# Kernel tuning notes

Hardware: AMD Instinct MI355X
Metric: run time of the kernel (lower is better)

The kernel has to match this reference:

```python
import jax, jax.numpy as jnp
import numpy as np

N_EXPERTS = 4
N_MODULES = 4
TOP_K = 2


def setup_inputs() -> dict:
    key = jax.random.key(0)
    k1, k2, k3 = jax.random.split(key, 3)
    B, d_model = 32768, 1024
    pooled_hidden = jax.random.normal(k1, (B, d_model), dtype=jnp.float32)
    # Xavier-uniform-ish scale for linear weights (torch Linear weight layout [out, in])
    lim_g = float(np.sqrt(6.0 / (d_model + d_model)))
    lim_r = float(np.sqrt(6.0 / (d_model + N_MODULES)))
    Wg = jax.random.uniform(k2, (d_model, d_model), jnp.float32, -lim_g, lim_g)
    Wr = jax.random.uniform(k3, (N_MODULES, d_model), jnp.float32, -lim_r, lim_r)
    return {"pooled_hidden": pooled_hidden, "Wg": Wg, "Wr": Wr}


def reference(pooled_hidden, Wg, Wr):
    # gated = g(h) = h @ Wg^T ; logits = gated @ Wr^T ; probs = softmax over modules
    gated = jnp.einsum("bd,ed->be", pooled_hidden, Wg)            # [B, d_model]
    logits = jnp.einsum("bd,md->bm", gated, Wr)                   # [B, n_modules]
    probs = jax.nn.softmax(logits, axis=-1)                        # [B, n_modules]

    # Vectorized replacement of the per-sample threshold loop:
    # prob > 0.5 -> first k experts get 1/k; else first max(1, k//2) get 1/that.
    n_lo = max(1, TOP_K // 2)
    eids = jnp.arange(N_EXPERTS)
    w_hi = jnp.where(eids < TOP_K, 1.0 / TOP_K, 0.0).astype(jnp.float32)   # [E]
    w_lo = jnp.where(eids < n_lo, 1.0 / n_lo, 0.0).astype(jnp.float32)     # [E]
    mask_hi = probs > 0.5                                          # [B, M]
    weights = jnp.where(mask_hi[:, :, None], w_hi, w_lo)          # [B, M, E]

    # Return per-module expert weights (Q, K, V, O order), each [B, n_experts]
    w = jnp.transpose(weights, (1, 0, 2))                          # [M, B, E]
    return (w[0], w[1], w[2], w[3])
```

## Files before the change

kernel.cpp:

```cpp
#include <hip/hip_runtime.h>

#define D_MODEL 1024
#define N_MOD   4
#define EB      32
#define ECHUNK  32
#define EPW     8

typedef float fx4 __attribute__((ext_vector_type(4)));

__global__ __launch_bounds__(256) void weff_partial_kernel(
    const fx4* __restrict__ Wg4,
    const float* __restrict__ Wr,
    fx4* __restrict__ partial4)
{
    const int t    = threadIdx.x;
    const int esub = t >> 6;
    const int d4   = t & 63;
    const int eb   = blockIdx.x;
    const int dc   = blockIdx.y;
    const int d4g  = dc * 64 + d4;
    const int e0   = eb * ECHUNK + esub * EPW;

    fx4 acc[N_MOD];
    #pragma unroll
    for (int m = 0; m < N_MOD; ++m) acc[m] = (fx4)(0.f);
    #pragma unroll
    for (int k = 0; k < EPW; ++k) {
        const int e = e0 + k;
        const fx4 wg = Wg4[e * 256 + d4g];
        #pragma unroll
        for (int m = 0; m < N_MOD; ++m)
            acc[m] += Wr[m * D_MODEL + e] * wg;
    }
    __shared__ fx4 red[4][N_MOD][64];
    #pragma unroll
    for (int m = 0; m < N_MOD; ++m) red[esub][m][d4] = acc[m];
    __syncthreads();
    const int m2 = t >> 6;
    const fx4 s = red[0][m2][d4] + red[1][m2][d4] + red[2][m2][d4] + red[3][m2][d4];
    partial4[(m2 * EB + eb) * 256 + d4g] = s;
}

__global__ __launch_bounds__(256) void weff_reduce_kernel(
    const float* __restrict__ partial, float* __restrict__ Weff)
{
    const int idx = blockIdx.x * 256 + threadIdx.x;
    const int m = idx >> 10;
    const int d = idx & (D_MODEL - 1);
    float s = 0.f;
    #pragma unroll
    for (int eb = 0; eb < EB; ++eb)
        s += partial[(m * EB + eb) * D_MODEL + d];
    Weff[idx] = s;
}

__global__ __launch_bounds__(256) void router_main_kernel(
    const float* __restrict__ h,
    const float* __restrict__ Weff,
    float* __restrict__ out,
    int B)
{
    const int lane = threadIdx.x & 63;
    const int wave = threadIdx.x >> 6;

    fx4 w4[N_MOD][4];
    const fx4* __restrict__ W4 = (const fx4*)Weff;
    #pragma unroll
    for (int m = 0; m < N_MOD; ++m)
        #pragma unroll
        for (int c = 0; c < 4; ++c)
            w4[m][c] = W4[m * 256 + c * 64 + lane];

    float4* __restrict__ out4 = (float4*)out;
    const int wid  = blockIdx.x * 4 + wave;
    const int step = gridDim.x * 4 * 8;

    for (int row0 = wid * 8; row0 < B; row0 += step) {
        unsigned mask = 0;
        #pragma unroll
        for (int i = 0; i < 8; ++i) {
            const int row = row0 + i;
            const fx4* __restrict__ h4 = (const fx4*)(h + (size_t)row * D_MODEL);
            fx4 v[4];
            #pragma unroll
            for (int c = 0; c < 4; ++c) v[c] = h4[c * 64 + lane];

            float acc[N_MOD] = {0.f, 0.f, 0.f, 0.f};
            #pragma unroll
            for (int c = 0; c < 4; ++c) {
                #pragma unroll
                for (int m = 0; m < N_MOD; ++m) {
                    acc[m] = fmaf(v[c].x, w4[m][c].x, acc[m]);
                    acc[m] = fmaf(v[c].y, w4[m][c].y, acc[m]);
                    acc[m] = fmaf(v[c].z, w4[m][c].z, acc[m]);
                    acc[m] = fmaf(v[c].w, w4[m][c].w, acc[m]);
                }
            }
            const bool b0 = lane & 1;
            float a  = (b0 ? acc[1] : acc[0]) + __shfl_xor(b0 ? acc[0] : acc[1], 1, 64);
            float cc = (b0 ? acc[3] : acc[2]) + __shfl_xor(b0 ? acc[2] : acc[3], 1, 64);
            const bool b1 = lane & 2;
            float r  = (b1 ? cc : a) + __shfl_xor(b1 ? a : cc, 2, 64);
            r += __shfl_xor(r, 4, 64);
            r += __shfl_xor(r, 8, 64);
            r += __shfl_xor(r, 16, 64);
            r += __shfl_xor(r, 32, 64);

            float mx = fmaxf(r, __shfl_xor(r, 1, 64));
            mx = fmaxf(mx, __shfl_xor(mx, 2, 64));
            const float ex = expf(r - mx);
            float S = ex + __shfl_xor(ex, 1, 64);
            S = S + __shfl_xor(S, 2, 64);
            const bool hi = (r == mx) && (S < 2.0f);
            mask |= (hi ? 1u : 0u) << i;
        }
        const int m = lane >> 3;
        const int rs = lane & 7;
        const unsigned mm = __shfl(mask, m, 64);
        if (lane < 32) {
            const bool hi = (mm >> rs) & 1;
            const float4 val = hi ? make_float4(0.5f, 0.5f, 0.f, 0.f)
                                  : make_float4(1.f, 0.f, 0.f, 0.f);
            out4[(size_t)m * B + row0 + rs] = val;
        }
    }
}

extern "C" void kernel_launch(void* const* d_in, const int* in_sizes, int n_in,
                              void* d_out, int out_size, void* d_ws, size_t ws_size,
                              hipStream_t stream) {
    const float* h  = (const float*)d_in[0];
    const fx4*   Wg = (const fx4*)d_in[1];
    const float* Wr = (const float*)d_in[2];
    float* out = (float*)d_out;

    const int B = in_sizes[0] / D_MODEL;

    float* Weff    = (float*)d_ws;
    fx4*   partial = (fx4*)((float*)d_ws + N_MOD * D_MODEL);

    dim3 g1(EB, 4);
    weff_partial_kernel<<<g1, 256, 0, stream>>>(Wg, Wr, partial);
    weff_reduce_kernel<<<(N_MOD * D_MODEL) / 256, 256, 0, stream>>>(
        (const float*)partial, Weff);

    const int grid = (B + 8 * 4 - 1) / (8 * 4);
    router_main_kernel<<<grid, 256, 0, stream>>>(h, Weff, out, B);
}
```

Baseline: 33.65 us.

## Fuse Weff reduction into partial kernel via last-block counter and software-pipeline row loads

```diff
diff --git a/kernel.cpp b/kernel.cpp
--- a/kernel.cpp
+++ b/kernel.cpp
@@ -8,10 +8,12 @@
 
 typedef float fx4 __attribute__((ext_vector_type(4)));
 
-__global__ __launch_bounds__(256) void weff_partial_kernel(
-    const fx4* __restrict__ Wg4,
+__global__ __launch_bounds__(256) void weff_stage_kernel(
+    const fx4*   __restrict__ Wg4,
     const float* __restrict__ Wr,
-    fx4* __restrict__ partial4)
+    fx4*         __restrict__ partial4,
+    fx4*         __restrict__ Weff4,
+    unsigned*    __restrict__ counters)
 {
     const int t    = threadIdx.x;
     const int esub = t >> 6;
@@ -37,21 +39,22 @@
     for (int m = 0; m < N_MOD; ++m) red[esub][m][d4] = acc[m];
     __syncthreads();
     const int m2 = t >> 6;
-    const fx4 s = red[0][m2][d4] + red[1][m2][d4] + red[2][m2][d4] + red[3][m2][d4];
-    partial4[(m2 * EB + eb) * 256 + d4g] = s;
-}
+    partial4[(m2 * EB + eb) * 256 + d4g] =
+        red[0][m2][d4] + red[1][m2][d4] + red[2][m2][d4] + red[3][m2][d4];
 
-__global__ __launch_bounds__(256) void weff_reduce_kernel(
-    const float* __restrict__ partial, float* __restrict__ Weff)
-{
-    const int idx = blockIdx.x * 256 + threadIdx.x;
-    const int m = idx >> 10;
-    const int d = idx & (D_MODEL - 1);
-    float s = 0.f;
-    #pragma unroll
-    for (int eb = 0; eb < EB; ++eb)
-        s += partial[(m * EB + eb) * D_MODEL + d];
-    Weff[idx] = s;
+    __threadfence();
+    __syncthreads();
+    __shared__ unsigned tick;
+    if (t == 0) tick = atomicAdd(&counters[dc], 1u);
+    __syncthreads();
+    if ((tick & 31u) == 31u) {
+        __threadfence();
+        fx4 s = (fx4)(0.f);
+        #pragma unroll
+        for (int eb2 = 0; eb2 < EB; ++eb2)
+            s += partial4[(m2 * EB + eb2) * 256 + d4g];
+        Weff4[m2 * 256 + d4g] = s;
+    }
 }
 
 __global__ __launch_bounds__(256) void router_main_kernel(
@@ -73,56 +76,78 @@
 
     float4* __restrict__ out4 = (float4*)out;
     const int wid  = blockIdx.x * 4 + wave;
-    const int step = gridDim.x * 4 * 8;
+    const int row0 = wid * 8;
+    if (row0 >= B) return;
 
-    for (int row0 = wid * 8; row0 < B; row0 += step) {
-        unsigned mask = 0;
+    const fx4* __restrict__ hb = (const fx4*)(h + (size_t)row0 * D_MODEL);
+
+    float acc[8][N_MOD];
+    #pragma unroll
+    for (int i = 0; i < 8; ++i)
         #pragma unroll
-        for (int i = 0; i < 8; ++i) {
-            const int row = row0 + i;
-            const fx4* __restrict__ h4 = (const fx4*)(h + (size_t)row * D_MODEL);
-            fx4 v[4];
-            #pragma unroll
-            for (int c = 0; c < 4; ++c) v[c] = h4[c * 64 + lane];
+        for (int m = 0; m < N_MOD; ++m) acc[i][m] = 0.f;
 
-            float acc[N_MOD] = {0.f, 0.f, 0.f, 0.f};
-            #pragma unroll
-            for (int c = 0; c < 4; ++c) {
-                #pragma unroll
-                for (int m = 0; m < N_MOD; ++m) {
-                    acc[m] = fmaf(v[c].x, w4[m][c].x, acc[m]);
-                    acc[m] = fmaf(v[c].y, w4[m][c].y, acc[m]);
-                    acc[m] = fmaf(v[c].z, w4[m][c].z, acc[m]);
-                    acc[m] = fmaf(v[c].w, w4[m][c].w, acc[m]);
-                }
-            }
-            const bool b0 = lane & 1;
-            float a  = (b0 ? acc[1] : acc[0]) + __shfl_xor(b0 ? acc[0] : acc[1], 1, 64);
-            float cc = (b0 ? acc[3] : acc[2]) + __shfl_xor(b0 ? acc[2] : acc[3], 1, 64);
-            const bool b1 = lane & 2;
-            float r  = (b1 ? cc : a) + __shfl_xor(b1 ? a : cc, 2, 64);
-            r += __shfl_xor(r, 4, 64);
-            r += __shfl_xor(r, 8, 64);
-            r += __shfl_xor(r, 16, 64);
-            r += __shfl_xor(r, 32, 64);
+    fx4 va[4], vb[4];
 
-            float mx = fmaxf(r, __shfl_xor(r, 1, 64));
-            mx = fmaxf(mx, __shfl_xor(mx, 2, 64));
-            const float ex = expf(r - mx);
-            float S = ex + __shfl_xor(ex, 1, 64);
-            S = S + __shfl_xor(S, 2, 64);
-            const bool hi = (r == mx) && (S < 2.0f);
-            mask |= (hi ? 1u : 0u) << i;
-        }
-        const int m = lane >> 3;
-        const int rs = lane & 7;
-        const unsigned mm = __shfl(mask, m, 64);
-        if (lane < 32) {
-            const bool hi = (mm >> rs) & 1;
-            const float4 val = hi ? make_float4(0.5f, 0.5f, 0.f, 0.f)
-                                  : make_float4(1.f, 0.f, 0.f, 0.f);
-            out4[(size_t)m * B + row0 + rs] = val;
-        }
+#define LOADV(dst, ri)                                             \
+    { const fx4* hp = hb + (ri) * 256;                             \
+      dst[0] = hp[0 * 64 + lane]; dst[1] = hp[1 * 64 + lane];      \
+      dst[2] = hp[2 * 64 + lane]; dst[3] = hp[3 * 64 + lane]; }
+
+#define FMAV(src, i)                                               \
+    { _Pragma("unroll")                                            \
+      for (int c = 0; c < 4; ++c) {                                \
+        _Pragma("unroll")                                          \
+        for (int m = 0; m < N_MOD; ++m) {                          \
+          acc[i][m] = fmaf(src[c].x, w4[m][c].x, acc[i][m]);       \
+          acc[i][m] = fmaf(src[c].y, w4[m][c].y, acc[i][m]);       \
+          acc[i][m] = fmaf(src[c].z, w4[m][c].z, acc[i][m]);       \
+          acc[i][m] = fmaf(src[c].w, w4[m][c].w, acc[i][m]);       \
+        } } }
+
+    LOADV(va, 0);
+    LOADV(vb, 1); FMAV(va, 0);
+    LOADV(va, 2); FMAV(vb, 1);
+    LOADV(vb, 3); FMAV(va, 2);
+    LOADV(va, 4); FMAV(vb, 3);
+    LOADV(vb, 5); FMAV(va, 4);
+    LOADV(va, 6); FMAV(vb, 5);
+    LOADV(vb, 7); FMAV(va, 6);
+    FMAV(vb, 7);
+#undef LOADV
+#undef FMAV
+
+    unsigned mask = 0;
+    #pragma unroll
+    for (int i = 0; i < 8; ++i) {
+        const bool b0 = lane & 1;
+        const float aa = (b0 ? acc[i][1] : acc[i][0])
+                       + __shfl_xor(b0 ? acc[i][0] : acc[i][1], 1, 64);
+        const float cc = (b0 ? acc[i][3] : acc[i][2])
+                       + __shfl_xor(b0 ? acc[i][2] : acc[i][3], 1, 64);
+        const bool b1 = lane & 2;
+        float r = (b1 ? cc : aa) + __shfl_xor(b1 ? aa : cc, 2, 64);
+        r += __shfl_xor(r, 4, 64);
+        r += __shfl_xor(r, 8, 64);
+        r += __shfl_xor(r, 16, 64);
+        r += __shfl_xor(r, 32, 64);
+        float mx = fmaxf(r, __shfl_xor(r, 1, 64));
+        mx = fmaxf(mx, __shfl_xor(mx, 2, 64));
+        const float ex = expf(r - mx);
+        float S = ex + __shfl_xor(ex, 1, 64);
+        S += __shfl_xor(S, 2, 64);
+        const bool hi = (r == mx) && (S < 2.0f);
+        mask |= (hi ? 1u : 0u) << i;
+    }
+
+    const int m  = lane >> 3;
+    const int rs = lane & 7;
+    const unsigned mm = __shfl(mask, m, 64);
+    if (lane < 32 && row0 + rs < B) {
+        const bool hi = (mm >> rs) & 1;
+        const float4 val = hi ? make_float4(0.5f, 0.5f, 0.f, 0.f)
+                              : make_float4(1.f, 0.f, 0.f, 0.f);
+        out4[(size_t)m * B + row0 + rs] = val;
     }
 }
 
@@ -136,13 +161,13 @@
 
     const int B = in_sizes[0] / D_MODEL;
 
-    float* Weff    = (float*)d_ws;
-    fx4*   partial = (fx4*)((float*)d_ws + N_MOD * D_MODEL);
+    float*    Weff     = (float*)d_ws;
+    fx4*      partial  = (fx4*)((float*)d_ws + N_MOD * D_MODEL);
+    unsigned* counters = (unsigned*)((char*)d_ws + 16 * 1024 + 512 * 1024);
 
     dim3 g1(EB, 4);
-    weff_partial_kernel<<<g1, 256, 0, stream>>>(Wg, Wr, partial);
-    weff_reduce_kernel<<<(N_MOD * D_MODEL) / 256, 256, 0, stream>>>(
-        (const float*)partial, Weff);
+    weff_stage_kernel<<<g1, 256, 0, stream>>>(Wg, Wr, partial, (fx4*)Weff,
+                                              counters);
 
     const int grid = (B + 8 * 4 - 1) / (8 * 4);
     router_main_kernel<<<grid, 256, 0, stream>>>(h, Weff, out, B);
```

New measurement: 47.45 us. +41.0%, slower.
